# Kernel optimization log

Measured on AMD Instinct MI355X. Metric: run time of the kernel, lower is better.

Reference implementation:

```python
import jax, jax.numpy as jnp
import numpy as np

B, L, N, D, H, FF, V, W, NL = 4, 1024, 4096, 1024, 16, 2752, 6, 16, 2
HD = D // H
EPS = 1e-6


def setup_inputs() -> dict:
    key = jax.random.key(0)
    ks = jax.random.split(key, 16)
    s = 0.02
    z_hat_l = jax.random.normal(ks[0], (B, L, D), jnp.float32)
    # one-hot merged->base source matrix: base position n was merged into token n*L//N
    assign = (jnp.arange(N) * L) // N                      # (N,)
    source = jnp.broadcast_to(jax.nn.one_hot(assign, L, dtype=jnp.float32).T, (B, L, N))
    p = lambda k, shp: jax.random.normal(k, shp, jnp.float32) * s
    return {
        'z_hat_l': z_hat_l,
        'source': source,
        'wq': p(ks[1], (NL, D, D)),
        'wk': p(ks[2], (NL, D, D)),
        'wv': p(ks[3], (NL, D, D)),
        'wo': p(ks[4], (NL, D, D)),
        'norm1_w': jnp.ones((NL, D), jnp.float32),
        'norm2_w': jnp.ones((NL, D), jnp.float32),
        'w1': p(ks[5], (NL, D, FF)),
        'w3': p(ks[6], (NL, D, FF)),
        'w2': p(ks[7], (NL, FF, D)),
        'final_norm_w': jnp.ones((D,), jnp.float32),
        'head_w': p(ks[8], (D, V)),
    }


def rmsnorm(x, w):
    ms = jnp.mean(jnp.square(x), axis=-1, keepdims=True)
    return x * jax.lax.rsqrt(ms + EPS) * w


def apply_rope(x, cos, sin):
    # x: (B,H,N,HD); cos/sin: (N, HD//2). Interleaved pair rotation.
    x1, x2 = x[..., 0::2], x[..., 1::2]
    r1 = x1 * cos - x2 * sin
    r2 = x1 * sin + x2 * cos
    return jnp.stack([r1, r2], axis=-1).reshape(x.shape)


def local_window_attn(q, k, v):
    # sliding window: query i attends keys j with |i-j| < W, via chunks of size W and 3W key window
    C = N // W
    qc = q.reshape(B, H, C, W, HD)
    kp = jnp.pad(k.reshape(B, H, C, W, HD), ((0, 0), (0, 0), (1, 1), (0, 0), (0, 0)))
    vp = jnp.pad(v.reshape(B, H, C, W, HD), ((0, 0), (0, 0), (1, 1), (0, 0), (0, 0)))
    kwin = jnp.concatenate([kp[:, :, i:i + C] for i in range(3)], axis=3)  # (B,H,C,3W,HD)
    vwin = jnp.concatenate([vp[:, :, i:i + C] for i in range(3)], axis=3)
    scores = jnp.einsum('bhcwd,bhcxd->bhcwx', qc, kwin) * (1.0 / np.sqrt(HD))
    w_idx = jnp.arange(W)
    x_idx = jnp.arange(3 * W)
    band = jnp.abs(w_idx[:, None] - x_idx[None, :] + W) < W            # (W,3W)
    kpos = (jnp.arange(C)[:, None] - 1) * W + x_idx[None, :]           # (C,3W)
    valid = (kpos >= 0) & (kpos < N)
    mask = band[None, :, :] & valid[:, None, :]                        # (C,W,3W)
    scores = jnp.where(mask, scores, -1e9)
    attn = jax.nn.softmax(scores, axis=-1)
    out = jnp.einsum('bhcwx,bhcxd->bhcwd', attn, vwin)
    return out.reshape(B, H, N, HD)


def reference(z_hat_l, source, wq, wk, wv, wo, norm1_w, norm2_w, w1, w3, w2, final_norm_w, head_w):
    # token unmerge: broadcast merged embeddings back to base positions
    z = jnp.einsum('bln,bld->bnd', source, z_hat_l)                    # (B,N,D)
    # RoPE tables for base positions arange(N)
    inv = 1.0 / (10000.0 ** (jnp.arange(0, HD, 2, dtype=jnp.float32) / HD))
    ang = jnp.arange(N, dtype=jnp.float32)[:, None] * inv[None, :]     # (N,HD/2)
    cos, sin = jnp.cos(ang), jnp.sin(ang)
    for i in range(NL):
        h = rmsnorm(z, norm1_w[i])
        q = (h @ wq[i]).reshape(B, N, H, HD).transpose(0, 2, 1, 3)
        k = (h @ wk[i]).reshape(B, N, H, HD).transpose(0, 2, 1, 3)
        v = (h @ wv[i]).reshape(B, N, H, HD).transpose(0, 2, 1, 3)
        q = apply_rope(q, cos, sin)
        k = apply_rope(k, cos, sin)
        o = local_window_attn(q, k, v)
        z = z + o.transpose(0, 2, 1, 3).reshape(B, N, D) @ wo[i]
        h = rmsnorm(z, norm2_w[i])
        z = z + (jax.nn.silu(h @ w1[i]) * (h @ w3[i])) @ w2[i]
    return rmsnorm(z, final_norm_w) @ head_w                           # (B,N,V)
```

## Files before the change

kernel.cpp:

```cpp
#include <hip/hip_runtime.h>
#include <hip/hip_bf16.h>
#include <math.h>

#define B_ 4
#define L_ 1024
#define N_ 4096
#define D_ 1024
#define H_ 16
#define FF_ 2752
#define NL_ 2
#define HD_ 64
#define M_ (B_*N_)

typedef short bf16x8 __attribute__((ext_vector_type(8)));
typedef float f32x4 __attribute__((ext_vector_type(4)));

__device__ __forceinline__ float bf2f(short s){
  unsigned int u = ((unsigned int)(unsigned short)s) << 16;
  union { unsigned int u; float f; } c; c.u = u; return c.f;
}
__device__ __forceinline__ short f2bf(float f){
  union { float f; unsigned int u; } c; c.f = f;
  unsigned int u = c.u;
  unsigned int r = (u + 0x7fffu + ((u >> 16) & 1u)) >> 16;
  return (short)r;
}

#define GPTR(p) ((const __attribute__((address_space(1))) void*)(p))
#define LPTR(p) ((__attribute__((address_space(3))) void*)(p))

__global__ __launch_bounds__(256) void gather2_kernel(const float* __restrict__ zh,
                                                      const float* __restrict__ src,
                                                      float* __restrict__ z,
                                                      float* __restrict__ cost,
                                                      float* __restrict__ sint){
  int bid = blockIdx.x;
  if (bid < 16384) {
    int idx = bid*256 + threadIdx.x;
    int d4 = idx & (D_/4 - 1);
    int n  = (idx >> 8) & (N_-1);
    int b  = idx >> 20;
    int l  = n >> 2;
    float s = src[((size_t)b*L_ + l)*N_ + n];
    float4 zv = *(const float4*)(zh + ((size_t)b*L_ + l)*D_ + d4*4);
    float4 o; o.x=zv.x*s; o.y=zv.y*s; o.z=zv.z*s; o.w=zv.w*s;
    *(float4*)(z + ((size_t)b*N_ + n)*D_ + d4*4) = o;
  } else {
    int idx = (bid-16384)*256 + threadIdx.x;
    int n = idx >> 5, j = idx & 31;
    float inv = __expf(-(float)j * (9.210340371976184f/32.0f));
    float ang = (float)n * inv;
    cost[idx] = cosf(ang);
    sint[idx] = sinf(ang);
  }
}

__global__ void tconv_kernel(const float* __restrict__ i0, const float* __restrict__ i1,
                             const float* __restrict__ i2, const float* __restrict__ i3,
                             short* __restrict__ o0, short* __restrict__ o1,
                             short* __restrict__ o2, short* __restrict__ o3,
                             int K, int Nc, int ldo, int bs, int gs, int go0, int gostep){
  __shared__ float tile[32][33];
  const float* in = (blockIdx.z==0) ? i0 : (blockIdx.z==1) ? i1 : (blockIdx.z==2) ? i2 : i3;
  short* out      = (blockIdx.z==0) ? o0 : (blockIdx.z==1) ? o1 : (blockIdx.z==2) ? o2 : o3;
  int go = go0 + (int)blockIdx.z * gostep;
  int k0 = blockIdx.x*32, r0 = blockIdx.y*32;
  int tx = threadIdx.x, ty = threadIdx.y;
  for (int i = ty; i < 32; i += 8)
    tile[i][tx] = in[(size_t)(k0+i)*Nc + r0 + tx];
  __syncthreads();
  for (int i = ty; i < 32; i += 8){
    int rr = r0 + i;
    int orow = (rr/bs)*gs + go + (rr % bs);
    out[(size_t)orow*ldo + k0 + tx] = f2bf(tile[tx][i]);
  }
}

__global__ __launch_bounds__(256) void rmsnorm_kernel(const float* __restrict__ z,
                                                      const float* __restrict__ w,
                                                      short* __restrict__ out){
  int row = blockIdx.x, tid = threadIdx.x;
  const float* x = z + (size_t)row*D_;
  float4 v = *(const float4*)(x + tid*4);
  float ss = v.x*v.x + v.y*v.y + v.z*v.z + v.w*v.w;
  #pragma unroll
  for (int off=32; off>0; off>>=1) ss += __shfl_down(ss, off, 64);
  __shared__ float red[4];
  if ((tid & 63) == 0) red[tid>>6] = ss;
  __syncthreads();
  float ms = (red[0]+red[1]+red[2]+red[3]) * (1.0f/D_);
  float rs = rsqrtf(ms + 1e-6f);
  float4 wv = *(const float4*)(w + tid*4);
  short4 o;
  o.x = f2bf(v.x*rs*wv.x); o.y = f2bf(v.y*rs*wv.y);
  o.z = f2bf(v.z*rs*wv.z); o.w = f2bf(v.w*rs*wv.w);
  *(short4*)(out + (size_t)row*D_ + tid*4) = o;
}

template<int EPI, int BN>
__global__ __launch_bounds__(256, 3) void gemm_bt_kernel(
    const short* __restrict__ A, int lda,
    const short* __restrict__ Bt, int ldb,
    void* __restrict__ Cout, int ldc, int K, int nx, int ny, int RG,
    const float* __restrict__ cosT, const float* __restrict__ sinT)
{
  constexpr int WC = (BN == 128) ? 2 : 1;
  constexpr int MI = (BN == 128) ? 4 : 2;
  constexpr int NI = 4;
  __shared__ short Al[128*64];
  __shared__ short Bl[BN*64];
  const int tid = threadIdx.x;
  const int wid = tid >> 6;
  const int lane = tid & 63;
  const int wr = wid / WC, wc = wid % WC;
  const int lrow = lane & 15;
  const int lk   = (lane >> 4) << 3;

  int bx, by;
  {
    const int lin = blockIdx.x;
    const int xcd = lin & 7;
    const int t   = lin >> 3;
    const int rpx = ny >> 3;
    const int gsz = RG * nx;
    int g   = t / gsz;
    int rem = t - g*gsz;
    int c   = rem / RG;
    int rl  = rem - c*RG;
    if (c & 1) rl = RG - 1 - rl;
    if (g & 1) c = nx - 1 - c;
    by = xcd*rpx + g*RG + rl;
    bx = c;
  }

  f32x4 acc[MI][NI];
  #pragma unroll
  for (int i=0;i<MI;i++)
    #pragma unroll
    for (int j=0;j<NI;j++) acc[i][j] = (f32x4){0.f,0.f,0.f,0.f};

  const size_t abase = (size_t)by * 128 * lda;
  const size_t bbase = (size_t)bx * BN  * ldb;

  for (int kt = 0; kt < K; kt += 64) {
    __syncthreads();
    #pragma unroll
    for (int r = 0; r < 4; ++r) {
      int l2 = (r<<8) + tid;
      int row = l2 >> 3, seg = l2 & 7;
      const short* ga = A + abase + (size_t)row*lda + kt + (seg<<3);
      int lbase = (r<<11) + (wid<<9);
      __builtin_amdgcn_global_load_lds(GPTR(ga), LPTR(Al + lbase), 16, 0, 0);
    }
    #pragma unroll
    for (int r = 0; r < BN/32; ++r) {
      int l2 = (r<<8) + tid;
      int row = l2 >> 3, seg = l2 & 7;
      const short* gb = Bt + bbase + (size_t)row*ldb + kt + (seg<<3);
      int lbase = (r<<11) + (wid<<9);
      __builtin_amdgcn_global_load_lds(GPTR(gb), LPTR(Bl + lbase), 16, 0, 0);
    }
    __syncthreads();

    #pragma unroll
    for (int kk = 0; kk < 64; kk += 32) {
      bf16x8 af[MI], bfr[NI];
      #pragma unroll
      for (int mi=0;mi<MI;mi++){
        int row = wr*(MI*16) + (mi<<4) + lrow;
        af[mi] = *(const bf16x8*)(Al + row*64 + kk + lk);
      }
      #pragma unroll
      for (int ni=0;ni<NI;ni++){
        int row = wc*(NI*16) + (ni<<4) + lrow;
        bfr[ni] = *(const bf16x8*)(Bl + row*64 + kk + lk);
      }
      #pragma unroll
      for (int mi=0;mi<MI;mi++)
        #pragma unroll
        for (int ni=0;ni<NI;ni++)
          acc[mi][ni] = __builtin_amdgcn_mfma_f32_16x16x32_bf16(af[mi], bfr[ni], acc[mi][ni], 0, 0, 0);
    }
  }

  const int crow0 = by*128 + wr*(MI*16);
  const int ccol0 = bx*BN  + wc*(NI*16);

  if (EPI == 2) {
    #pragma unroll
    for (int mi=0;mi<MI;mi++){
      #pragma unroll
      for (int p=0;p<NI/2;p++){
        int fcol = (ccol0>>1) + (p<<4) + lrow;
        int rowb = crow0 + (mi<<4) + ((lane>>4)<<2);
        #pragma unroll
        for (int v=0;v<4;v++){
          float g = acc[mi][2*p][v], u = acc[mi][2*p+1][v];
          float a = g * u / (1.0f + __expf(-g));
          ((short*)Cout)[(size_t)(rowb+v)*ldc + fcol] = f2bf(a);
        }
      }
    }
  } else if (EPI == 3) {
    #pragma unroll
    for (int mi=0;mi<MI;mi++){
      #pragma unroll
      for (int ni=0;ni<NI;ni++){
        int col  = ccol0 + (ni<<4) + lrow;
        int rowb = crow0 + (mi<<4) + ((lane>>4)<<2);
        bool qk = (col < 2048);
        int jhd = (col >> 1) & 31;
        #pragma unroll
        for (int v=0;v<4;v++){
          float val = acc[mi][ni][v];
          int row = rowb + v;
          int trow = row & (N_-1);
          float partner = __shfl_xor(val, 1, 64);
          if (qk) {
            float cc = cosT[(trow<<5)+jhd], ssn = sinT[(trow<<5)+jhd];
            float r = (lane & 1) ? (val*cc + partner*ssn) : (val*cc - partner*ssn);
            val = (col < 1024) ? r*0.125f : r;
          }
          ((short*)Cout)[(size_t)row*ldc + col] = f2bf(val);
        }
      }
    }
  } else {
    #pragma unroll
    for (int mi=0;mi<MI;mi++){
      #pragma unroll
      for (int ni=0;ni<NI;ni++){
        int col  = ccol0 + (ni<<4) + lrow;
        int rowb = crow0 + (mi<<4) + ((lane>>4)<<2);
        #pragma unroll
        for (int v=0;v<4;v++){
          float val = acc[mi][ni][v];
          int row = rowb + v;
          if (EPI == 0) ((short*)Cout)[(size_t)row*ldc + col] = f2bf(val);
          else          ((float*)Cout)[(size_t)row*ldc + col] += val;
        }
      }
    }
  }
}

#define QB_ 128
__global__ __launch_bounds__(256, 2) void attn_kernel(const short* __restrict__ qkv,
                                                      short* __restrict__ o){
  __shared__ float Kf[160*68];
  __shared__ short Vl[160*72];
  const int h  = blockIdx.y;
  const int n0 = blockIdx.x * QB_;
  const int lo = n0 & ~(N_-1);
  const int hi = lo + N_ - 1;
  const int tid = threadIdx.x;

  for (int i = tid; i < 1280; i += 256){
    int r = i >> 3, g = i & 7;
    int m = n0 - 16 + r;
    int mc = m < lo ? lo : (m > hi ? hi : m);
    bf16x8 kv = *(const bf16x8*)(qkv + (size_t)mc*3072 + 1024 + h*64 + (g<<3));
    bf16x8 vv = *(const bf16x8*)(qkv + (size_t)mc*3072 + 2048 + h*64 + (g<<3));
    int sw = ((r>>3)&3)<<1;
    float4 lof, hif;
    lof.x=bf2f(kv[0]); lof.y=bf2f(kv[1]); lof.z=bf2f(kv[2]); lof.w=bf2f(kv[3]);
    hif.x=bf2f(kv[4]); hif.y=bf2f(kv[5]); hif.z=bf2f(kv[6]); hif.w=bf2f(kv[7]);
    *(float4*)(Kf + r*68 + (((2*g)   ^ sw)<<2)) = lof;
    *(float4*)(Kf + r*68 + (((2*g+1) ^ sw)<<2)) = hif;
    *(bf16x8*)(Vl + r*72 + (g<<3)) = vv;
  }
  __syncthreads();

  const int q  = tid >> 1;
  const int dh = tid & 1;
  const int nc = n0 + q;

  const short* qp = qkv + (size_t)nc*3072 + h*64 + dh*32;
  float qr[32];
  #pragma unroll
  for (int i=0;i<4;i++){
    bf16x8 qv = *(const bf16x8*)(qp + i*8);
    #pragma unroll
    for (int t=0;t<8;t++) qr[i*8+t] = bf2f(qv[t]);
  }

  float sc[31];
  float mx = -1e30f;
  #pragma unroll
  for (int t=0;t<31;t++){
    int m = nc - 15 + t;
    int r = q + 1 + t;
    int sw = ((r>>3)&3)<<1;
    const float* kp = Kf + r*68;
    float dot = 0.f;
    #pragma unroll
    for (int i=0;i<8;i++){
      float4 kv4 = *(const float4*)(kp + (((dh*8+i)^sw)<<2));
      dot += qr[i*4+0]*kv4.x + qr[i*4+1]*kv4.y + qr[i*4+2]*kv4.z + qr[i*4+3]*kv4.w;
    }
    dot += __shfl_xor(dot, 1, 64);
    bool valid = (m>=lo) && (m<=hi);
    sc[t] = valid ? dot : -1e30f;
    mx = fmaxf(mx, sc[t]);
  }
  float sum = 0.f;
  #pragma unroll
  for (int t=0;t<31;t++){ sc[t] = __expf(sc[t]-mx); sum += sc[t]; }
  float inv = 1.0f/sum;

  float ov[32];
  #pragma unroll
  for (int i=0;i<32;i++) ov[i]=0.f;
  #pragma unroll
  for (int t=0;t<31;t++){
    const short* vp = Vl + (q + 1 + t)*72 + dh*32;
    float p = sc[t]*inv;
    #pragma unroll
    for (int i=0;i<4;i++){
      bf16x8 vv = *(const bf16x8*)(vp + i*8);
      #pragma unroll
      for (int u=0;u<8;u++) ov[i*8+u] += p * bf2f(vv[u]);
    }
  }
  short* op = o + (size_t)nc*1024 + h*64 + dh*32;
  #pragma unroll
  for (int i=0;i<4;i++){
    bf16x8 wv;
    #pragma unroll
    for (int u=0;u<8;u++) wv[u] = f2bf(ov[i*8+u]);
    *(bf16x8*)(op + i*8) = wv;
  }
}

__global__ __launch_bounds__(256) void head_kernel(const float* __restrict__ z,
                                                   const float* __restrict__ fw,
                                                   const float* __restrict__ hw,
                                                   float* __restrict__ out){
  int row = blockIdx.x, tid = threadIdx.x;
  const float* x = z + (size_t)row*D_;
  float4 v = *(const float4*)(x + tid*4);
  float ss = v.x*v.x + v.y*v.y + v.z*v.z + v.w*v.w;
  #pragma unroll
  for (int off=32; off>0; off>>=1) ss += __shfl_down(ss, off, 64);
  __shared__ float red[4];
  if ((tid & 63) == 0) red[tid>>6] = ss;
  __syncthreads();
  float ms = (red[0]+red[1]+red[2]+red[3]) * (1.0f/D_);
  float rs = rsqrtf(ms + 1e-6f);
  float4 wv = *(const float4*)(fw + tid*4);
  float h0 = v.x*rs*wv.x, h1 = v.y*rs*wv.y, h2 = v.z*rs*wv.z, h3 = v.w*rs*wv.w;
  float p[6];
  #pragma unroll
  for (int t=0;t<6;t++){
    const float* hp = hw + (size_t)(tid*4)*6 + t;
    p[t] = h0*hp[0] + h1*hp[6] + h2*hp[12] + h3*hp[18];
  }
  #pragma unroll
  for (int t=0;t<6;t++)
    #pragma unroll
    for (int off=32; off>0; off>>=1) p[t] += __shfl_down(p[t], off, 64);
  __shared__ float wred[4][6];
  if ((tid & 63) == 0)
    #pragma unroll
    for (int t=0;t<6;t++) wred[tid>>6][t] = p[t];
  __syncthreads();
  if (tid < 6)
    out[(size_t)row*6 + tid] = wred[0][tid]+wred[1][tid]+wred[2][tid]+wred[3][tid];
}

extern "C" void kernel_launch(void* const* d_in, const int* in_sizes, int n_in,
                              void* d_out, int out_size, void* d_ws, size_t ws_size,
                              hipStream_t stream)
{
  (void)in_sizes; (void)n_in; (void)out_size;
  const float* z_hat  = (const float*)d_in[0];
  const float* source = (const float*)d_in[1];
  const float* wq  = (const float*)d_in[2];
  const float* wk  = (const float*)d_in[3];
  const float* wvp = (const float*)d_in[4];
  const float* wo  = (const float*)d_in[5];
  const float* n1w = (const float*)d_in[6];
  const float* n2w = (const float*)d_in[7];
  const float* w1  = (const float*)d_in[8];
  const float* w3  = (const float*)d_in[9];
  const float* w2  = (const float*)d_in[10];
  const float* fnw = (const float*)d_in[11];
  const float* hw  = (const float*)d_in[12];
  float* out = (float*)d_out;
  char* ws = (char*)d_ws;
  dim3 tb(32,8);

  const bool fullM = (ws_size >= 219283456ULL);

  if (fullM) {
    float* z     = (float*)(ws);
    short* h     = (short*)(ws + 67108864);
    short* qkv   = (short*)(ws + 100663296);
    short* act   = qkv;
    short* qkvW  = (short*)(ws + 201326592);
    short* woW   = (short*)(ws + 207618048);
    short* w13W  = (short*)(ws + 201326592);
    short* w2W   = (short*)(ws + 212598784);
    float* cosT  = (float*)(ws + 218234880);
    float* sinT  = (float*)(ws + 218759168);

    gather2_kernel<<<16896,256,0,stream>>>(z_hat, source, z, cosT, sinT);

    for (int l=0; l<NL_; l++){
      size_t wofs = (size_t)l*D_*D_;
      tconv_kernel<<<dim3(32,32,4),tb,0,stream>>>(
          wq + wofs, wk + wofs, wvp + wofs, wo + wofs,
          qkvW, qkvW + 1024*1024, qkvW + 2048*1024, woW,
          1024,1024,1024, 64,64, 0,0);
      rmsnorm_kernel<<<M_,256,0,stream>>>(z, n1w + l*D_, h);
      gemm_bt_kernel<3,128><<<3072,256,0,stream>>>(h,1024, qkvW,1024, qkv,3072, 1024, 24,128,16, cosT, sinT);
      attn_kernel<<<dim3(M_/QB_,H_),256,0,stream>>>(qkv, h);
      gemm_bt_kernel<1,64><<<2048,256,0,stream>>>(h,1024, woW,1024, z,1024, 1024, 16,128,16, cosT, sinT);
      tconv_kernel<<<dim3(32,86,2),tb,0,stream>>>(
          w1 + (size_t)l*D_*FF_, w3 + (size_t)l*D_*FF_, w1, w1,
          w13W, w13W, w13W, w13W,
          1024,2752,1024, 16,32, 0,16);
      tconv_kernel<<<dim3(86,32,1),tb,0,stream>>>(
          w2 + (size_t)l*FF_*D_, w2, w2, w2,
          w2W, w2W, w2W, w2W,
          2752,1024,2752, 64,64, 0,0);
      rmsnorm_kernel<<<M_,256,0,stream>>>(z, n2w + l*D_, h);
      gemm_bt_kernel<2,128><<<5504,256,0,stream>>>(h,1024, w13W,1024, act,2752, 1024, 43,128,16, cosT, sinT);
      gemm_bt_kernel<1,64><<<2048,256,0,stream>>>(act,2752, w2W,2752, z,1024, 2752, 16,128,4, cosT, sinT);
    }
    head_kernel<<<M_,256,0,stream>>>(z, fnw, hw, out);

  } else {
    float* z     = (float*)(ws);
    short* h_b   = (short*)(ws + 67108864);
    short* qkv_b = (short*)(ws + 75497472);
    short* act_b = qkv_b;
    short* o_b   = (short*)(ws + 100663296);
    short* qkvW  = (short*)(ws + 109051904);
    short* woW   = (short*)(ws + 115343360);
    short* w13W  = (short*)(ws + 109051904);
    short* w2W   = (short*)(ws + 120324096);
    float* cosT  = (float*)(ws + 125960192);
    float* sinT  = (float*)(ws + 126484480);

    gather2_kernel<<<16896,256,0,stream>>>(z_hat, source, z, cosT, sinT);

    for (int l=0; l<NL_; l++){
      size_t wofs = (size_t)l*D_*D_;
      tconv_kernel<<<dim3(32,32,4),tb,0,stream>>>(
          wq + wofs, wk + wofs, wvp + wofs, wo + wofs,
          qkvW, qkvW + 1024*1024, qkvW + 2048*1024, woW,
          1024,1024,1024, 64,64, 0,0);
      for (int b=0; b<B_; b++){
        float* zb = z + (size_t)b*N_*D_;
        rmsnorm_kernel<<<N_,256,0,stream>>>(zb, n1w + l*D_, h_b);
        gemm_bt_kernel<3,128><<<768,256,0,stream>>>(h_b,1024, qkvW,1024, qkv_b,3072, 1024, 24,32,4, cosT, sinT);
        attn_kernel<<<dim3(N_/QB_,H_),256,0,stream>>>(qkv_b, o_b);
        gemm_bt_kernel<1,64><<<512,256,0,stream>>>(o_b,1024, woW,1024, zb,1024, 1024, 16,32,4, cosT, sinT);
      }
      tconv_kernel<<<dim3(32,86,2),tb,0,stream>>>(
          w1 + (size_t)l*D_*FF_, w3 + (size_t)l*D_*FF_, w1, w1,
          w13W, w13W, w13W, w13W,
          1024,2752,1024, 16,32, 0,16);
      tconv_kernel<<<dim3(86,32,1),tb,0,stream>>>(
          w2 + (size_t)l*FF_*D_, w2, w2, w2,
          w2W, w2W, w2W, w2W,
          2752,1024,2752, 64,64, 0,0);
      for (int b=0; b<B_; b++){
        float* zb = z + (size_t)b*N_*D_;
        rmsnorm_kernel<<<N_,256,0,stream>>>(zb, n2w + l*D_, h_b);
        gemm_bt_kernel<2,128><<<1376,256,0,stream>>>(h_b,1024, w13W,1024, act_b,2752, 1024, 43,32,4, cosT, sinT);
        gemm_bt_kernel<1,64><<<512,256,0,stream>>>(act_b,2752, w2W,2752, zb,1024, 2752, 16,32,4, cosT, sinT);
      }
    }
    head_kernel<<<M_,256,0,stream>>>(z, fnw, hw, out);
  }
}
```

Measured before the change: 1.518 ms.

## Add 256x128 eight-wave triple-buffered GEMM for the fused W1/W3 SwiGLU projection

Adds a new GEMM kernel with 512 threads, 256x128 output tiles, three LDS stages fed by direct global-to-LDS loads, XOR-swizzled LDS rows and an interleaved four-phase MFMA schedule with priority bumps. It also uses an XCD-aware tile ordering. The W1/W3 gate-up projection with the SiLU-multiply epilogue now runs on this kernel instead of the 128x128 one. The aim is higher MFMA utilisation and better overlap of loads with compute, at the cost of more LDS per block and lower occupancy.

```diff
diff --git a/kernel.cpp b/kernel.cpp
--- a/kernel.cpp
+++ b/kernel.cpp
@@ -97,6 +97,198 @@
   *(short4*)(out + (size_t)row*D_ + tid*4) = o;
 }
 
+template<int EPI>
+__global__ __launch_bounds__(512, 2) void gemm8p_kernel(
+    const short* __restrict__ A, int lda,
+    const short* __restrict__ Bt, int ldb,
+    void* __restrict__ Cout, int ldc, int K, int nx, int ny, int RG)
+{
+  __shared__ __align__(16) short Al[3][256*64];
+  __shared__ __align__(16) short Bl[3][128*64];
+  const int tid  = threadIdx.x;
+  const int lane = tid & 63;
+  const int wid  = tid >> 6;
+  const int wm   = wid >> 1;
+  const int wn   = wid & 1;
+  const int lrow = lane & 15;
+  const int lk   = (lane >> 4) << 3;
+  const int swd  = (lrow & 7) << 3;
+
+  int bx, by;
+  {
+    const int lin = blockIdx.x;
+    const int xcd = lin & 7;
+    const int t   = lin >> 3;
+    const int rpx = ny >> 3;
+    const int gsz = RG * nx;
+    int g   = t / gsz;
+    int rem = t - g*gsz;
+    int c   = rem / RG;
+    int rl  = rem - c*RG;
+    if (c & 1) rl = RG - 1 - rl;
+    if (g & 1) c = nx - 1 - c;
+    by = xcd*rpx + g*RG + rl;
+    bx = c;
+  }
+
+  const short* Ab = A  + (size_t)by*256*lda;
+  const short* Bb = Bt + (size_t)bx*128*ldb;
+
+  auto SA = [&](int t, int s, int r){
+    int chunk = r*512 + tid;
+    int row = chunk >> 3;
+    int scol = ((chunk & 7) << 3) ^ ((row & 7) << 3);
+    __builtin_amdgcn_global_load_lds(GPTR(Ab + (size_t)row*lda + (t<<6) + scol),
+                                     LPTR(&Al[s][chunk<<3]), 16, 0, 0);
+  };
+  auto SB = [&](int t, int s, int r){
+    int chunk = r*512 + tid;
+    int row = chunk >> 3;
+    int scol = ((chunk & 7) << 3) ^ ((row & 7) << 3);
+    __builtin_amdgcn_global_load_lds(GPTR(Bb + (size_t)row*ldb + (t<<6) + scol),
+                                     LPTR(&Bl[s][chunk<<3]), 16, 0, 0);
+  };
+
+  f32x4 acc[4][4];
+  #pragma unroll
+  for (int i=0;i<4;i++)
+    #pragma unroll
+    for (int j=0;j<4;j++) acc[i][j] = (f32x4){0.f,0.f,0.f,0.f};
+
+  bf16x8 aL[2][2], aH[2][2], bL[2][2], bH[2][2];
+
+  const int NT = K >> 6;
+  SA(0,0,0);SA(0,0,1);SA(0,0,2);SA(0,0,3);SB(0,0,0);SB(0,0,1);
+  SA(1,1,0);SA(1,1,1);SA(1,1,2);SA(1,1,3);SB(1,1,0);SB(1,1,1);
+  asm volatile("s_waitcnt vmcnt(6)" ::: "memory");
+  __builtin_amdgcn_sched_barrier(0);
+  __builtin_amdgcn_s_barrier();
+
+  int slot = 0;
+  for (int t = 0; t < NT; ++t){
+    const short* As = Al[slot];
+    const short* Bs = Bl[slot];
+    int ns = slot + 2; if (ns >= 3) ns -= 3;
+    const bool st = (t + 2 < NT);
+    const int arow = (wm<<6) + lrow;
+    const int brow = (wn<<6) + lrow;
+
+    #pragma unroll
+    for (int mi=0;mi<2;mi++)
+      #pragma unroll
+      for (int kk=0;kk<2;kk++)
+        aL[mi][kk] = *(const bf16x8*)(As + (arow + mi*16)*64 + (((kk<<5)+lk)^swd));
+    #pragma unroll
+    for (int ni=0;ni<2;ni++)
+      #pragma unroll
+      for (int kk=0;kk<2;kk++)
+        bL[ni][kk] = *(const bf16x8*)(Bs + (brow + ni*16)*64 + (((kk<<5)+lk)^swd));
+    if (st){ SA(t+2,ns,0); SA(t+2,ns,1); }
+    __builtin_amdgcn_sched_barrier(0);
+    __builtin_amdgcn_s_barrier();
+    __builtin_amdgcn_sched_barrier(0);
+    __builtin_amdgcn_s_setprio(1);
+    #pragma unroll
+    for (int kk=0;kk<2;kk++)
+      #pragma unroll
+      for (int mi=0;mi<2;mi++)
+        #pragma unroll
+        for (int ni=0;ni<2;ni++)
+          acc[mi][ni] = __builtin_amdgcn_mfma_f32_16x16x32_bf16(aL[mi][kk], bL[ni][kk], acc[mi][ni], 0,0,0);
+    __builtin_amdgcn_s_setprio(0);
+    __builtin_amdgcn_sched_barrier(0);
+    __builtin_amdgcn_s_barrier();
+
+    #pragma unroll
+    for (int mi=0;mi<2;mi++)
+      #pragma unroll
+      for (int kk=0;kk<2;kk++)
+        aH[mi][kk] = *(const bf16x8*)(As + (arow + 32 + mi*16)*64 + (((kk<<5)+lk)^swd));
+    if (st){ SA(t+2,ns,2); SA(t+2,ns,3); }
+    __builtin_amdgcn_sched_barrier(0);
+    __builtin_amdgcn_s_barrier();
+    __builtin_amdgcn_sched_barrier(0);
+    __builtin_amdgcn_s_setprio(1);
+    #pragma unroll
+    for (int kk=0;kk<2;kk++)
+      #pragma unroll
+      for (int mi=0;mi<2;mi++)
+        #pragma unroll
+        for (int ni=0;ni<2;ni++)
+          acc[2+mi][ni] = __builtin_amdgcn_mfma_f32_16x16x32_bf16(aH[mi][kk], bL[ni][kk], acc[2+mi][ni], 0,0,0);
+    __builtin_amdgcn_s_setprio(0);
+    __builtin_amdgcn_sched_barrier(0);
+    __builtin_amdgcn_s_barrier();
+
+    #pragma unroll
+    for (int ni=0;ni<2;ni++)
+      #pragma unroll
+      for (int kk=0;kk<2;kk++)
+        bH[ni][kk] = *(const bf16x8*)(Bs + (brow + 32 + ni*16)*64 + (((kk<<5)+lk)^swd));
+    if (st){ SB(t+2,ns,0); SB(t+2,ns,1); }
+    __builtin_amdgcn_sched_barrier(0);
+    __builtin_amdgcn_s_barrier();
+    __builtin_amdgcn_sched_barrier(0);
+    __builtin_amdgcn_s_setprio(1);
+    #pragma unroll
+    for (int kk=0;kk<2;kk++)
+      #pragma unroll
+      for (int mi=0;mi<2;mi++)
+        #pragma unroll
+        for (int ni=0;ni<2;ni++)
+          acc[2+mi][2+ni] = __builtin_amdgcn_mfma_f32_16x16x32_bf16(aH[mi][kk], bH[ni][kk], acc[2+mi][2+ni], 0,0,0);
+    __builtin_amdgcn_s_setprio(0);
+    __builtin_amdgcn_sched_barrier(0);
+    __builtin_amdgcn_s_barrier();
+
+    __builtin_amdgcn_s_setprio(1);
+    #pragma unroll
+    for (int kk=0;kk<2;kk++)
+      #pragma unroll
+      for (int mi=0;mi<2;mi++)
+        #pragma unroll
+        for (int ni=0;ni<2;ni++)
+          acc[mi][2+ni] = __builtin_amdgcn_mfma_f32_16x16x32_bf16(aL[mi][kk], bH[ni][kk], acc[mi][2+ni], 0,0,0);
+    __builtin_amdgcn_s_setprio(0);
+    if (st) asm volatile("s_waitcnt vmcnt(6)" ::: "memory");
+    else    asm volatile("s_waitcnt vmcnt(0)" ::: "memory");
+    __builtin_amdgcn_sched_barrier(0);
+    __builtin_amdgcn_s_barrier();
+    slot = (slot == 2) ? 0 : slot + 1;
+  }
+
+  const int crow0 = by*256 + (wm<<6);
+  const int ccol0 = bx*128 + (wn<<6);
+  if (EPI == 2) {
+    #pragma unroll
+    for (int mi=0;mi<4;mi++){
+      #pragma unroll
+      for (int p=0;p<2;p++){
+        int fcol = (ccol0>>1) + (p<<4) + lrow;
+        int rowb = crow0 + (mi<<4) + ((lane>>4)<<2);
+        #pragma unroll
+        for (int v=0;v<4;v++){
+          float g = acc[mi][2*p][v], u = acc[mi][2*p+1][v];
+          float a = g * u / (1.0f + __expf(-g));
+          ((short*)Cout)[(size_t)(rowb+v)*ldc + fcol] = f2bf(a);
+        }
+      }
+    }
+  } else {
+    #pragma unroll
+    for (int mi=0;mi<4;mi++){
+      #pragma unroll
+      for (int ni=0;ni<4;ni++){
+        int col  = ccol0 + (ni<<4) + lrow;
+        int rowb = crow0 + (mi<<4) + ((lane>>4)<<2);
+        #pragma unroll
+        for (int v=0;v<4;v++)
+          ((short*)Cout)[(size_t)(rowb+v)*ldc + col] = f2bf(acc[mi][ni][v]);
+      }
+    }
+  }
+}
+
 template<int EPI, int BN>
 __global__ __launch_bounds__(256, 3) void gemm_bt_kernel(
     const short* __restrict__ A, int lda,
@@ -425,7 +617,7 @@
           w2W, w2W, w2W, w2W,
           2752,1024,2752, 64,64, 0,0);
       rmsnorm_kernel<<<M_,256,0,stream>>>(z, n2w + l*D_, h);
-      gemm_bt_kernel<2,128><<<5504,256,0,stream>>>(h,1024, w13W,1024, act,2752, 1024, 43,128,16, cosT, sinT);
+      gemm8p_kernel<2><<<2752,512,0,stream>>>(h,1024, w13W,1024, act,2752, 1024, 43,64,4);
       gemm_bt_kernel<1,64><<<2048,256,0,stream>>>(act,2752, w2W,2752, z,1024, 2752, 16,128,4, cosT, sinT);
     }
     head_kernel<<<M_,256,0,stream>>>(z, fnw, hw, out);
```

After: 1.534 ms. No clear change (+1.0%).
